# Performance work log

Measured on AMD Instinct MI355X. Metric: run time of the kernel, lower is better.

Reference implementation:

```python
import jax, jax.numpy as jnp
import numpy as np

N_NODES = 100000


def _gat_conv(x, edge_index, W, att_src, att_dst, bias, concat):
    """PyG-style GATConv (eval mode, self-loops already in edge_index).
    x: [N, F_in], W: [F_in, H*C], att_*: [H, C], bias: [H*C] or [C].
    """
    N = x.shape[0]
    H, C = att_src.shape
    xl = (x @ W).reshape(N, H, C)                      # [N, H, C]
    a_src = jnp.einsum('nhc,hc->nh', xl, att_src)      # [N, H]
    a_dst = jnp.einsum('nhc,hc->nh', xl, att_dst)      # [N, H]
    src, dst = edge_index[0], edge_index[1]
    e = jax.nn.leaky_relu(a_src[src] + a_dst[dst], negative_slope=0.2)  # [E, H]
    # segment softmax over incoming edges per destination node
    e_max = jax.ops.segment_max(e, dst, num_segments=N)                 # [N, H]
    e_exp = jnp.exp(e - e_max[dst])                                     # [E, H]
    denom = jax.ops.segment_sum(e_exp, dst, num_segments=N)             # [N, H]
    alpha = e_exp / (denom[dst] + 1e-16)                                # [E, H]
    msg = xl[src] * alpha[:, :, None]                                   # [E, H, C]
    out = jax.ops.segment_sum(msg, dst, num_segments=N)                 # [N, H, C]
    out = out.reshape(N, H * C) if concat else out.mean(axis=1)
    return out + bias


def setup_inputs() -> dict:
    key = jax.random.key(0)
    ks = jax.random.split(key, 12)
    in_dim, hidden, heads, out_dim = 128, 16, 8, 64
    E = 1600000
    x = jax.random.normal(ks[0], (N_NODES, in_dim), dtype=jnp.float32)
    edge_index = jax.random.randint(ks[1], (2, E), 0, N_NODES, dtype=jnp.int32)
    s1 = 1.0 / np.sqrt(in_dim)
    s2 = 1.0 / np.sqrt(hidden * heads)
    return {
        'x': x,
        'edge_index': edge_index,
        'W1': jax.random.normal(ks[2], (in_dim, heads * hidden), dtype=jnp.float32) * s1,
        'att_src1': jax.random.normal(ks[3], (heads, hidden), dtype=jnp.float32) * 0.1,
        'att_dst1': jax.random.normal(ks[4], (heads, hidden), dtype=jnp.float32) * 0.1,
        'b1': jnp.zeros((heads * hidden,), dtype=jnp.float32),
        'W2': jax.random.normal(ks[5], (heads * hidden, out_dim), dtype=jnp.float32) * s2,
        'att_src2': jax.random.normal(ks[6], (1, out_dim), dtype=jnp.float32) * 0.1,
        'att_dst2': jax.random.normal(ks[7], (1, out_dim), dtype=jnp.float32) * 0.1,
        'b2': jnp.zeros((out_dim,), dtype=jnp.float32),
    }


def reference(x, edge_index, W1, att_src1, att_dst1, b1, W2, att_src2, att_dst2, b2):
    N = x.shape[0]
    # PyG GATConv default add_self_loops=True
    loops = jnp.tile(jnp.arange(N, dtype=edge_index.dtype), (2, 1))
    ei = jnp.concatenate([edge_index, loops], axis=1)
    h = _gat_conv(x, ei, W1, att_src1, att_dst1, b1, concat=True)
    h = jax.nn.elu(h)
    # dropout is identity in eval mode
    out = _gat_conv(h, ei, W2, att_src2, att_dst2, b2, concat=False)
    return out
```

## Files before the change

kernel.cpp:

```cpp
#include <hip/hip_runtime.h>
#include <cmath>

typedef _Float16 half8 __attribute__((ext_vector_type(8)));
typedef float f32x4 __attribute__((ext_vector_type(4)));

#define CAP 48

__device__ __forceinline__ float elu1(float v) {
    return v > 0.f ? v : (__expf(v) - 1.f);
}

__global__ __launch_bounds__(256) void k_build(
    const int* __restrict__ src, const int* __restrict__ dst,
    int* __restrict__ cnt, int* __restrict__ sorted, int E, int M, int npc, int SB,
    const float* __restrict__ x, const float* __restrict__ W,
    const float* __restrict__ att_s, const float* __restrict__ att_d,
    _Float16* __restrict__ xlh, float* __restrict__ a_s, float* __restrict__ a_d, int N)
{
    __shared__ _Float16 Wt[128 * 72];
    int t = threadIdx.x;

    if ((int)blockIdx.x < SB) {
        int color = blockIdx.x & 7;
        int lo = color * npc, hi = lo + npc;
        int nb = SB >> 3;
        size_t stride = (size_t)nb * 256;
        for (size_t e = (size_t)(blockIdx.x >> 3) * 256 + t; e < (size_t)M; e += stride) {
            int s, d;
            if (e < (size_t)E) { s = src[e]; d = dst[e]; } else { s = (int)(e - E); d = s; }
            if (d >= lo && d < hi) {
                int pos = atomicAdd(&cnt[d], 1);
                if (pos < CAP) sorted[(size_t)d * CAP + pos] = s;
            }
        }
        return;
    }

    int bx = blockIdx.x - SB;
    int wave = t >> 6, lane = t & 63;
    int cl = lane & 15, quad = lane >> 4;
    int arow = bx * 64 + wave * 16 + cl;
    int rr = arow < N ? arow : N - 1;

    half8 af[4];
#pragma unroll
    for (int ks = 0; ks < 4; ks++) {
        const float4* p = (const float4*)(x + (size_t)rr * 128 + ks * 32 + quad * 8);
        float4 A = p[0], B = p[1];
        af[ks][0] = (_Float16)A.x; af[ks][1] = (_Float16)A.y;
        af[ks][2] = (_Float16)A.z; af[ks][3] = (_Float16)A.w;
        af[ks][4] = (_Float16)B.x; af[ks][5] = (_Float16)B.y;
        af[ks][6] = (_Float16)B.z; af[ks][7] = (_Float16)B.w;
    }

    f32x4 acc[8];
#pragma unroll
    for (int nt = 0; nt < 8; nt++) acc[nt] = (f32x4){0.f, 0.f, 0.f, 0.f};

#pragma unroll
    for (int h = 0; h < 2; h++) {
        if (h) __syncthreads();
        for (int i = t; i < 128 * 64; i += 256) {
            int k0 = i >> 7, n = i & 127;
            Wt[n * 72 + k0] = (_Float16)W[(size_t)(h * 64 + k0) * 128 + n];
        }
        __syncthreads();
#pragma unroll
        for (int nt = 0; nt < 8; nt++) {
            int n = nt * 16 + cl;
#pragma unroll
            for (int ks2 = 0; ks2 < 2; ks2++) {
                half8 bf = *(const half8*)&Wt[n * 72 + ks2 * 32 + quad * 8];
                acc[nt] = __builtin_amdgcn_mfma_f32_16x16x32_f16(
                    af[h * 2 + ks2], bf, acc[nt], 0, 0, 0);
            }
        }
    }

    float asl[8], adl[8];
#pragma unroll
    for (int nt = 0; nt < 8; nt++) {
        asl[nt] = att_s[nt * 16 + cl];
        adl[nt] = att_d[nt * 16 + cl];
    }

    int rbase = bx * 64 + wave * 16 + quad * 4;
#pragma unroll
    for (int r = 0; r < 4; r++) {
        int orow = rbase + r;
        bool ok = orow < N;
#pragma unroll
        for (int nt = 0; nt < 8; nt++) {
            float v = acc[nt][r];
            if (ok) xlh[(size_t)orow * 128 + nt * 16 + cl] = (_Float16)v;
        }
#pragma unroll
        for (int nt = 0; nt < 8; nt++) {
            float ps = acc[nt][r] * asl[nt];
            float pd = acc[nt][r] * adl[nt];
            ps += __shfl_xor(ps, 1); ps += __shfl_xor(ps, 2);
            ps += __shfl_xor(ps, 4); ps += __shfl_xor(ps, 8);
            pd += __shfl_xor(pd, 1); pd += __shfl_xor(pd, 2);
            pd += __shfl_xor(pd, 4); pd += __shfl_xor(pd, 8);
            if (ok && cl == 0) {
                a_s[(size_t)orow * 8 + nt] = ps;
                a_d[(size_t)orow * 8 + nt] = pd;
            }
        }
    }
}

__global__ __launch_bounds__(256) void k_agg1_gemm2(
    const int* __restrict__ cnt, const int* __restrict__ ss,
    const float* __restrict__ as, const float* __restrict__ ad,
    const _Float16* __restrict__ xlh, const float* __restrict__ b1,
    const float* __restrict__ W2,
    const float* __restrict__ att_s2, const float* __restrict__ att_d2,
    _Float16* __restrict__ xl2h, float* __restrict__ a_s2, float* __restrict__ a_d2, int N)
{
    __shared__ _Float16 W2t[64 * 136];
    __shared__ _Float16 Ht[32 * 136];
    __shared__ float asb[2][32], adb[2][32];

    int t = threadIdx.x;

    for (int i = t; i < 128 * 64; i += 256) {
        int k = i >> 6, n = i & 63;
        W2t[n * 136 + k] = (_Float16)W2[i];
    }

    int ln = t >> 3;
    int g = blockIdx.x * 32 + ln;
    int lane8 = t & 7;
    int c = lane8 * 16;
    {
        int gg = g < N ? g : N - 1;
        int deg = cnt[gg]; deg = deg < CAP ? deg : CAP;
        int start = gg * CAP, end = start + deg;
        float adv = ad[(size_t)gg * 8 + lane8];

        float l = 0.f;
        float acc[16];
#pragma unroll
        for (int j = 0; j < 16; j++) acc[j] = 0.f;

        int i = start;
        for (; i + 2 <= end; i += 2) {
            int s0 = ss[i], s1 = ss[i + 1];
            float a0 = as[(size_t)s0 * 8 + lane8];
            float a1 = as[(size_t)s1 * 8 + lane8];
            const _Float16* p0 = xlh + (size_t)s0 * 128 + c;
            const _Float16* p1 = xlh + (size_t)s1 * 128 + c;
            half8 x0a = *(const half8*)p0, x0b = *(const half8*)(p0 + 8);
            half8 x1a = *(const half8*)p1, x1b = *(const half8*)(p1 + 8);
            float v0 = a0 + adv; v0 = v0 > 0.f ? v0 : 0.2f * v0;
            float v1 = a1 + adv; v1 = v1 > 0.f ? v1 : 0.2f * v1;
            float w0 = __expf(v0), w1 = __expf(v1);
            l += w0 + w1;
#pragma unroll
            for (int j = 0; j < 8; j++) {
                acc[j]     += (float)x0a[j] * w0 + (float)x1a[j] * w1;
                acc[j + 8] += (float)x0b[j] * w0 + (float)x1b[j] * w1;
            }
        }
        if (i < end) {
            int s0 = ss[i];
            float v0 = as[(size_t)s0 * 8 + lane8] + adv;
            v0 = v0 > 0.f ? v0 : 0.2f * v0;
            float w0 = __expf(v0);
            l += w0;
            const _Float16* p0 = xlh + (size_t)s0 * 128 + c;
            half8 x0a = *(const half8*)p0, x0b = *(const half8*)(p0 + 8);
#pragma unroll
            for (int j = 0; j < 8; j++) {
                acc[j]     += (float)x0a[j] * w0;
                acc[j + 8] += (float)x0b[j] * w0;
            }
        }
        float inv = 1.f / (l + 1e-16f);
        float4 bq[4];
        bq[0] = *(const float4*)(b1 + c);
        bq[1] = *(const float4*)(b1 + c + 4);
        bq[2] = *(const float4*)(b1 + c + 8);
        bq[3] = *(const float4*)(b1 + c + 12);
        const float* bb = (const float*)bq;
        half8 o0, o1;
#pragma unroll
        for (int j = 0; j < 8; j++) {
            o0[j] = (_Float16)elu1(acc[j] * inv + bb[j]);
            o1[j] = (_Float16)elu1(acc[j + 8] * inv + bb[j + 8]);
        }
        *(half8*)&Ht[ln * 136 + c] = o0;
        *(half8*)&Ht[ln * 136 + c + 8] = o1;
    }
    __syncthreads();

    int wave = t >> 6, lane = t & 63;
    int cl = lane & 15, quad = lane >> 4;
    int rt = wave >> 1;
    int half = wave & 1;

    half8 af[4];
#pragma unroll
    for (int ks = 0; ks < 4; ks++)
        af[ks] = *(const half8*)&Ht[(rt * 16 + cl) * 136 + ks * 32 + quad * 8];

    f32x4 acc2[2];
    acc2[0] = (f32x4){0.f, 0.f, 0.f, 0.f};
    acc2[1] = (f32x4){0.f, 0.f, 0.f, 0.f};
    float asl[2], adl[2];
#pragma unroll
    for (int ntl = 0; ntl < 2; ntl++) {
        int n = (half * 2 + ntl) * 16 + cl;
        asl[ntl] = att_s2[n];
        adl[ntl] = att_d2[n];
#pragma unroll
        for (int ks = 0; ks < 4; ks++) {
            half8 bf = *(const half8*)&W2t[n * 136 + ks * 32 + quad * 8];
            acc2[ntl] = __builtin_amdgcn_mfma_f32_16x16x32_f16(af[ks], bf, acc2[ntl], 0, 0, 0);
        }
    }

#pragma unroll
    for (int r = 0; r < 4; r++) {
        int lrow = rt * 16 + quad * 4 + r;
        int orow = blockIdx.x * 32 + lrow;
        bool ok = orow < N;
        float ps = 0.f, pd = 0.f;
#pragma unroll
        for (int ntl = 0; ntl < 2; ntl++) {
            float v = acc2[ntl][r];
            if (ok) xl2h[(size_t)orow * 64 + (half * 2 + ntl) * 16 + cl] = (_Float16)v;
            ps += v * asl[ntl];
            pd += v * adl[ntl];
        }
        ps += __shfl_xor(ps, 1); ps += __shfl_xor(ps, 2);
        ps += __shfl_xor(ps, 4); ps += __shfl_xor(ps, 8);
        pd += __shfl_xor(pd, 1); pd += __shfl_xor(pd, 2);
        pd += __shfl_xor(pd, 4); pd += __shfl_xor(pd, 8);
        if (cl == 0) { asb[half][lrow] = ps; adb[half][lrow] = pd; }
    }
    __syncthreads();
    if (t < 32) {
        int orow = blockIdx.x * 32 + t;
        if (orow < N) {
            a_s2[orow] = asb[0][t] + asb[1][t];
            a_d2[orow] = adb[0][t] + adb[1][t];
        }
    }
}

__global__ __launch_bounds__(256) void k_agg2(
    const int* __restrict__ cnt, const int* __restrict__ ss,
    const float* __restrict__ as, const float* __restrict__ ad,
    const _Float16* __restrict__ xlh, const float* __restrict__ b2,
    float* __restrict__ out, int N)
{
    int t = threadIdx.x;
    int g = (blockIdx.x * 256 + t) >> 3;
    if (g >= N) return;
    int lane = t & 7;
    int c = lane * 8;
    int deg = cnt[g]; deg = deg < CAP ? deg : CAP;
    int start = g * CAP, end = start + deg;
    float adv = ad[g];

    float l = 0.f;
    float acc[8];
#pragma unroll
    for (int j = 0; j < 8; j++) acc[j] = 0.f;

    int i = start;
    for (; i + 4 <= end; i += 4) {
        int s0 = ss[i], s1 = ss[i + 1], s2 = ss[i + 2], s3 = ss[i + 3];
        float a0 = as[s0], a1 = as[s1], a2 = as[s2], a3 = as[s3];
        half8 x0 = *(const half8*)(xlh + (size_t)s0 * 64 + c);
        half8 x1 = *(const half8*)(xlh + (size_t)s1 * 64 + c);
        half8 x2 = *(const half8*)(xlh + (size_t)s2 * 64 + c);
        half8 x3 = *(const half8*)(xlh + (size_t)s3 * 64 + c);
        float v0 = a0 + adv; v0 = v0 > 0.f ? v0 : 0.2f * v0;
        float v1 = a1 + adv; v1 = v1 > 0.f ? v1 : 0.2f * v1;
        float v2 = a2 + adv; v2 = v2 > 0.f ? v2 : 0.2f * v2;
        float v3 = a3 + adv; v3 = v3 > 0.f ? v3 : 0.2f * v3;
        float w0 = __expf(v0), w1 = __expf(v1), w2 = __expf(v2), w3 = __expf(v3);
        l += (w0 + w1) + (w2 + w3);
#pragma unroll
        for (int j = 0; j < 8; j++)
            acc[j] += ((float)x0[j] * w0 + (float)x1[j] * w1)
                    + ((float)x2[j] * w2 + (float)x3[j] * w3);
    }
    for (; i < end; i++) {
        int s0 = ss[i];
        float v0 = as[s0] + adv;
        v0 = v0 > 0.f ? v0 : 0.2f * v0;
        float w0 = __expf(v0);
        l += w0;
        half8 x0 = *(const half8*)(xlh + (size_t)s0 * 64 + c);
#pragma unroll
        for (int j = 0; j < 8; j++) acc[j] += (float)x0[j] * w0;
    }
    float inv = 1.f / (l + 1e-16f);
    float4 b0 = *(const float4*)(b2 + c);
    float4 b4 = *(const float4*)(b2 + c + 4);
    float bb[8] = {b0.x, b0.y, b0.z, b0.w, b4.x, b4.y, b4.z, b4.w};
    float4 o0, o1;
    o0.x = acc[0] * inv + bb[0];
    o0.y = acc[1] * inv + bb[1];
    o0.z = acc[2] * inv + bb[2];
    o0.w = acc[3] * inv + bb[3];
    o1.x = acc[4] * inv + bb[4];
    o1.y = acc[5] * inv + bb[5];
    o1.z = acc[6] * inv + bb[6];
    o1.w = acc[7] * inv + bb[7];
    *(float4*)(out + (size_t)g * 64 + c) = o0;
    *(float4*)(out + (size_t)g * 64 + c + 4) = o1;
}

extern "C" void kernel_launch(void* const* d_in, const int* in_sizes, int n_in,
                              void* d_out, int out_size, void* d_ws, size_t ws_size,
                              hipStream_t stream) {
    const float* x   = (const float*)d_in[0];
    const int*   ei  = (const int*)  d_in[1];
    const float* W1  = (const float*)d_in[2];
    const float* as1 = (const float*)d_in[3];
    const float* ad1 = (const float*)d_in[4];
    const float* b1  = (const float*)d_in[5];
    const float* W2  = (const float*)d_in[6];
    const float* as2 = (const float*)d_in[7];
    const float* ad2 = (const float*)d_in[8];
    const float* b2  = (const float*)d_in[9];

    const int N = in_sizes[0] / 128;
    const int E = in_sizes[1] / 2;
    const int M = E + N;
    const int npc = (N + 7) / 8;
    const int SB = ((M + 256 * 8 - 1) / (256 * 8)) * 8;
    const int GB = (N + 63) / 64;
    const int* src = ei;
    const int* dst = ei + E;

    float* ws    = (float*)d_ws;
    _Float16* xl1h = (_Float16*)ws;
    float* as1v  = ws   + (size_t)N * 64;
    float* ad1v  = as1v + (size_t)N * 8;
    _Float16* xl2h = (_Float16*)(ad1v + (size_t)N * 8);
    float* as2v  = ad1v + (size_t)N * 8 + (size_t)N * 32;
    float* ad2v  = as2v + (size_t)N;
    int*   cnt   = (int*)(ad2v + (size_t)N);
    int*   sorted= cnt + (size_t)N;
    float* out   = (float*)d_out;

    size_t need = ((size_t)N * (115 + CAP)) * 4;
    if (ws_size < need) return;

    hipMemsetAsync(cnt, 0, (size_t)N * 4, stream);

    k_build<<<SB + GB, 256, 0, stream>>>(
        src, dst, cnt, sorted, E, M, npc, SB,
        x, W1, as1, ad1, xl1h, as1v, ad1v, N);

    k_agg1_gemm2<<<(N + 31) / 32, 256, 0, stream>>>(
        cnt, sorted, as1v, ad1v, xl1h, b1, W2, as2, ad2, xl2h, as2v, ad2v, N);

    k_agg2 <<<(int)(((size_t)N * 8 + 255) / 256), 256, 0, stream>>>(
        cnt, sorted, as2v, ad2v, xl2h, b2, out, N);
}
```

Measured before the change: 336.2 us.

## Interleave scatter and GEMM block groups in fused build kernel, batch edge loads

Reorganizes the k_build grid so GEMM block groups are interleaved among the edge-bucketing groups at a fixed ratio instead of all running after the scatter blocks. The intent is for compute-bound GEMM work and atomic-bound scatter work to co-reside on the CUs and overlap. The scatter loop is also restructured to issue four independent edge loads before the corresponding atomics, doing up to eight edges per thread, which raises memory-level parallelism. The index mapping is more complex, and the hardcoded eight iterations assume the grid covers M edges exactly in that count.

```diff
diff --git a/kernel.cpp b/kernel.cpp
--- a/kernel.cpp
+++ b/kernel.cpp
@@ -12,31 +12,63 @@
 
 __global__ __launch_bounds__(256) void k_build(
     const int* __restrict__ src, const int* __restrict__ dst,
-    int* __restrict__ cnt, int* __restrict__ sorted, int E, int M, int npc, int SB,
+    int* __restrict__ cnt, int* __restrict__ sorted,
+    int E, int M, int npc, int SGRP, int GGRP, int R, int GB,
     const float* __restrict__ x, const float* __restrict__ W,
     const float* __restrict__ att_s, const float* __restrict__ att_d,
     _Float16* __restrict__ xlh, float* __restrict__ a_s, float* __restrict__ a_d, int N)
 {
     __shared__ _Float16 Wt[128 * 72];
     int t = threadIdx.x;
-
-    if ((int)blockIdx.x < SB) {
-        int color = blockIdx.x & 7;
+    int bid = (int)blockIdx.x;
+    int grp = bid >> 3;
+
+    bool isg;
+    int sgrp, gg;
+    if (R >= 2) {
+        int k = grp / R;
+        isg = ((grp - k * R) == (R - 1)) && (k < GGRP);
+        int cg = k < GGRP ? k : GGRP;
+        sgrp = grp - cg;
+        gg = k;
+    } else {
+        isg = grp >= SGRP;
+        sgrp = grp;
+        gg = grp - SGRP;
+    }
+
+    if (!isg) {
+        int color = bid & 7;
         int lo = color * npc, hi = lo + npc;
-        int nb = SB >> 3;
-        size_t stride = (size_t)nb * 256;
-        for (size_t e = (size_t)(blockIdx.x >> 3) * 256 + t; e < (size_t)M; e += stride) {
-            int s, d;
-            if (e < (size_t)E) { s = src[e]; d = dst[e]; } else { s = (int)(e - E); d = s; }
-            if (d >= lo && d < hi) {
-                int pos = atomicAdd(&cnt[d], 1);
-                if (pos < CAP) sorted[(size_t)d * CAP + pos] = s;
+        size_t stride = (size_t)SGRP * 256;
+        size_t e0 = (size_t)sgrp * 256 + t;
+#pragma unroll
+        for (int half = 0; half < 2; half++) {
+            int sv[4], dv[4];
+#pragma unroll
+            for (int it = 0; it < 4; it++) {
+                size_t e = e0 + (size_t)(half * 4 + it) * stride;
+                int s = 0, d = -1;
+                if (e < (size_t)M) {
+                    if (e < (size_t)E) { s = src[e]; d = dst[e]; }
+                    else               { s = (int)(e - E); d = s; }
+                }
+                sv[it] = s; dv[it] = d;
+            }
+#pragma unroll
+            for (int it = 0; it < 4; it++) {
+                int d = dv[it];
+                if (d >= lo && d < hi) {
+                    int pos = atomicAdd(&cnt[d], 1);
+                    if (pos < CAP) sorted[(size_t)d * CAP + pos] = sv[it];
+                }
             }
         }
         return;
     }
 
-    int bx = blockIdx.x - SB;
+    int bx = gg * 8 + (bid & 7);
+    if (bx >= GB) return;
     int wave = t >> 6, lane = t & 63;
     int cl = lane & 15, quad = lane >> 4;
     int arow = bx * 64 + wave * 16 + cl;
@@ -334,8 +366,11 @@
     const int E = in_sizes[1] / 2;
     const int M = E + N;
     const int npc = (N + 7) / 8;
-    const int SB = ((M + 256 * 8 - 1) / (256 * 8)) * 8;
+    const int SGRP = (M + 256 * 8 - 1) / (256 * 8);
     const int GB = (N + 63) / 64;
+    const int GGRP = (GB + 7) / 8;
+    const int Tg = SGRP + GGRP;
+    int R = GGRP > 0 ? Tg / GGRP : 0;
     const int* src = ei;
     const int* dst = ei + E;
 
@@ -355,8 +390,8 @@
 
     hipMemsetAsync(cnt, 0, (size_t)N * 4, stream);
 
-    k_build<<<SB + GB, 256, 0, stream>>>(
-        src, dst, cnt, sorted, E, M, npc, SB,
+    k_build<<<Tg * 8, 256, 0, stream>>>(
+        src, dst, cnt, sorted, E, M, npc, SGRP, GGRP, R, GB,
         x, W1, as1, ad1, xl1h, as1v, ad1v, N);
 
     k_agg1_gemm2<<<(N + 31) / 32, 256, 0, stream>>>(
```

Result: faster. 323.4 us (-3.8%).
